# Kernel optimization log

Hardware: AMD Instinct MI355X
Metric: run time of the kernel (lower is better)

## Reference

```python
import jax, jax.numpy as jnp
import numpy as np

T, B, V, L_MAX = 1000, 64, 1024, 64
BLANK = 0
LAMBDA_FAIR = 0.5
NUM_GROUPS = 2
NEG = jnp.float32(-1e30)  # finite stand-in for -inf (nan-safe under vjp)


def setup_inputs() -> dict:
    key = jax.random.key(0)
    k1, k2, k3, k4, k5 = jax.random.split(key, 5)
    # caller passes log-softmaxed acoustic model outputs [T, B, V]
    log_probs = jax.nn.log_softmax(jax.random.normal(k1, (T, B, V), jnp.float32), axis=-1)
    # flat concatenated targets; values in [1, V) (blank=0 excluded, as in real CTC targets)
    targets = jax.random.randint(k2, (B * L_MAX,), 1, V, dtype=jnp.int32)
    input_lengths = jax.random.randint(k3, (B,), T // 2, T + 1, dtype=jnp.int32)
    target_lengths = jax.random.randint(k4, (B,), 0, L_MAX, dtype=jnp.int32)  # 0 allowed (tests t_len==0 branch)
    group_ids = jax.random.randint(k5, (B,), 0, NUM_GROUPS, dtype=jnp.int32)
    return {"log_probs": log_probs, "targets": targets, "input_lengths": input_lengths,
            "target_lengths": target_lengths, "group_ids": group_ids}


def _ctc_per_sample(log_probs, targets, input_lengths, target_lengths):
    """Batched CTC NLL (reduction='none'), log-domain alpha recursion."""
    Tn, Bn, Vn = log_probs.shape
    # unflatten targets per sample: offsets = exclusive cumsum of target_lengths
    offsets = jnp.cumsum(target_lengths) - target_lengths                      # [B]
    pos = offsets[:, None] + jnp.arange(L_MAX)[None, :]                        # [B, L]
    valid = jnp.arange(L_MAX)[None, :] < target_lengths[:, None]
    tgt = jnp.where(valid, targets[jnp.clip(pos, 0, targets.shape[0] - 1)], BLANK)  # [B, L]

    S = 2 * L_MAX + 1  # extended label sequence with interleaved blanks
    ext = jnp.full((Bn, S), BLANK, dtype=targets.dtype).at[:, 1::2].set(tgt)   # [B, S]
    # emission log-probs gathered once: em[t, b, s] = log_probs[t, b, ext[b, s]]
    em = jnp.take_along_axis(log_probs, jnp.broadcast_to(ext[None], (Tn, Bn, S)), axis=2)

    ext_m2 = jnp.pad(ext[:, :-2], ((0, 0), (2, 0)), constant_values=BLANK)
    s_idx = jnp.arange(S)
    allow_skip = (s_idx[None, :] >= 2) & (ext != BLANK) & (ext != ext_m2)      # [B, S]

    def end_ll(alpha):
        last = 2 * target_lengths                                              # index of final blank
        a1 = jnp.take_along_axis(alpha, last[:, None], axis=1)[:, 0]
        a2 = jnp.take_along_axis(alpha, jnp.clip(last - 1, 0)[:, None], axis=1)[:, 0]
        return jnp.logaddexp(a1, jnp.where(target_lengths > 0, a2, NEG))

    alpha0 = jnp.full((Bn, S), NEG).at[:, 0].set(em[0, :, 0])
    alpha0 = alpha0.at[:, 1].set(jnp.where(target_lengths > 0, em[0, :, 1], NEG))
    final0 = jnp.where(input_lengths == 1, end_ll(alpha0), NEG)

    def step(carry, xs):
        alpha, final = carry
        em_t, t = xs
        sh1 = jnp.concatenate([jnp.full((Bn, 1), NEG), alpha[:, :-1]], axis=1)
        sh2 = jnp.concatenate([jnp.full((Bn, 2), NEG), alpha[:, :-2]], axis=1)
        alpha = jnp.logaddexp(jnp.logaddexp(alpha, sh1),
                              jnp.where(allow_skip, sh2, NEG)) + em_t
        final = jnp.where(t == input_lengths - 1, end_ll(alpha), final)
        return (alpha, final), None

    (_, final), _ = jax.lax.scan(step, (alpha0, final0), (em[1:], jnp.arange(1, Tn)))
    loss = jnp.where(target_lengths > 0, -final, 0.0)   # t_len==0 -> loss 0 (as in original)
    loss = jnp.where(loss < 1e29, loss, 0.0)            # zero_infinity=True
    return loss


def reference(log_probs, targets, input_lengths, target_lengths, group_ids):
    per_sample = _ctc_per_sample(log_probs, targets, input_lengths, target_lengths)  # [B]
    base_loss = per_sample.mean()
    ones = jnp.ones_like(per_sample)
    counts = jax.ops.segment_sum(ones, group_ids, num_segments=NUM_GROUPS)
    sums = jax.ops.segment_sum(per_sample, group_ids, num_segments=NUM_GROUPS)
    group_means = sums / jnp.maximum(counts, 1.0)
    fairness_penalty = jnp.var(group_means, ddof=1)     # torch .var() is unbiased
    total = base_loss + LAMBDA_FAIR * fairness_penalty
    return total, base_loss, fairness_penalty
```

## Files before the change

kernel.cpp:

```cpp
#include <hip/hip_runtime.h>

#define T_ 1000
#define B_ 64
#define V_ 1024
#define NEGF (-1e30f)
#define LOG2E_ 1.4426950408889634f
#define LN2_ 0.6931471805599453f
#define P0C 1.4405f
#define P1C (-0.64178f)
#define P2C 0.20128f

__device__ __forceinline__ float ex2(float x) { return __builtin_amdgcn_exp2f(x); }
__device__ __forceinline__ float lg2(float x) { return __builtin_amdgcn_logf(x); }
__device__ __forceinline__ float rlane(float x, int l) {
    return __int_as_float(__builtin_amdgcn_readlane(__float_as_int(x), l));
}
#define FENCE_ __builtin_amdgcn_sched_barrier(0)

__device__ __forceinline__ void load_tgt(const int* __restrict__ targets,
                                         const int* __restrict__ tlen,
                                         int b, int lane, int& tg, int& L) {
    int tl = tlen[lane];
    L = __shfl(tl, b);
    int v = (lane < b) ? tl : 0;
    for (int off = 32; off; off >>= 1) v += __shfl_xor(v, off);
    tg = (lane < L) ? targets[v + lane] : 0;
}

__global__ __launch_bounds__(64) void ctc_fb_k(const float* __restrict__ lp,
                                               const int* __restrict__ targets,
                                               const int* __restrict__ tlen,
                                               const int* __restrict__ ilen,
                                               float* __restrict__ aw) {
    int blk = blockIdx.x, lane = threadIdx.x;
    bool isFwd = blk < B_;
    int b = isFwd ? blk : blk - B_;
    int tg, L;
    load_tgt(targets, tlen, b, lane, tg, L);
    int Tin = ilen[b], Te = Tin - 1;
    int M = Te >> 1;
    int tgp = __shfl_up(tg, 1);
    bool skip1 = (lane >= 1) && (tg != 0) && (tg != tgp);
    int col = (lane == 63) ? 0 : tg;
    int idx = (b << 10) + col;
    float* awb = aw + b * 256;

    if (isFwd) {
        bool is16 = (lane == 16), is32 = (lane == 32), is48 = (lane == 48);
        float a0 = NEGF, a1 = NEGF;
        auto ldG = [&](int g, float4& S) {
            int t0 = 4 * g;
            int ta = t0 < M ? t0 : M, tb2 = t0 + 1 < M ? t0 + 1 : M;
            int tc = t0 + 2 < M ? t0 + 2 : M, td = t0 + 3 < M ? t0 + 3 : M;
            S.x = (lp + ((size_t)ta << 16))[idx];
            S.y = (lp + ((size_t)tb2 << 16))[idx];
            S.z = (lp + ((size_t)tc << 16))[idx];
            S.w = (lp + ((size_t)td << 16))[idx];
        };
        auto shr1 = [&](float x) -> float {
            float v15 = rlane(x, 15), v31 = rlane(x, 31), v47 = rlane(x, 47);
            float bval = is16 ? v15 : (is32 ? v31 : (is48 ? v47 : NEGF));
            return __int_as_float(__builtin_amdgcn_update_dpp(
                __float_as_int(bval), __float_as_int(x), 0x111, 0xF, 0xF, false));
        };
        auto step = [&](float xb, float xe) {
            float p1m = shr1(a1);
            float d0 = a0 - p1m;
            float m0 = fmaxf(a0, p1m);
            float u = ex2(-fabsf(d0));
            float h = fmaf(u, P2C, P1C);
            h = fmaf(u, h, P0C);
            float U = fmaf(u, h, m0);
            float na0 = U + xb;
            float w = skip1 ? U : a0;
            float d1 = a1 - w;
            float m1 = fmaxf(a1, w);
            float v = ex2(-fabsf(d1));
            float h1 = fmaf(v, P2C, P1C);
            h1 = fmaf(v, h1, P0C);
            float na1 = fmaf(v, h1, m1 + xe);
            a0 = na0; a1 = na1;
        };
        if (M >= 35) {
            float4 S0, S1, S2, S3, S4, S5, S6, S7;
            ldG(0, S0); ldG(1, S1); ldG(2, S2); ldG(3, S3);
            ldG(4, S4); ldG(5, S5); ldG(6, S6); ldG(7, S7);
            FENCE_;
            {
                float e0 = S0.x * LOG2E_, e1 = S0.y * LOG2E_;
                float e2 = S0.z * LOG2E_, e3 = S0.w * LOG2E_;
                a0 = (lane == 0) ? rlane(e0, 63) : NEGF;
                a1 = (lane == 0 && L > 0) ? e0 : NEGF;
                step(rlane(e1, 63), e1); step(rlane(e2, 63), e2); step(rlane(e3, 63), e3);
                ldG(8, S0);
                FENCE_;
            }
#define SUBF_F(S, G) do {                                                      \
            float e0_ = S.x * LOG2E_, e1_ = S.y * LOG2E_;                      \
            float e2_ = S.z * LOG2E_, e3_ = S.w * LOG2E_;                      \
            float b0_ = rlane(e0_, 63), b1_ = rlane(e1_, 63);                  \
            float b2_ = rlane(e2_, 63), b3_ = rlane(e3_, 63);                  \
            step(b0_, e0_); step(b1_, e1_); step(b2_, e2_); step(b3_, e3_);    \
            ldG((G) + 8, S);                                                   \
            FENCE_;                                                            \
        } while (0)
            SUBF_F(S1, 1); SUBF_F(S2, 2); SUBF_F(S3, 3); SUBF_F(S4, 4);
            SUBF_F(S5, 5); SUBF_F(S6, 6); SUBF_F(S7, 7);
            int c = 1;
            for (; 32 * c + 31 <= M; ++c) {
                int g0 = 8 * c;
                SUBF_F(S0, g0 + 0); SUBF_F(S1, g0 + 1); SUBF_F(S2, g0 + 2); SUBF_F(S3, g0 + 3);
                SUBF_F(S4, g0 + 4); SUBF_F(S5, g0 + 5); SUBF_F(S6, g0 + 6); SUBF_F(S7, g0 + 7);
            }
#undef SUBF_F
            int tb = 32 * c;
#define SUBT_F(S, T0) do {                                                     \
            float e0_ = S.x * LOG2E_, e1_ = S.y * LOG2E_;                      \
            float e2_ = S.z * LOG2E_, e3_ = S.w * LOG2E_;                      \
            float b0_ = rlane(e0_, 63), b1_ = rlane(e1_, 63);                  \
            float b2_ = rlane(e2_, 63), b3_ = rlane(e3_, 63);                  \
            if ((T0) + 0 <= M) step(b0_, e0_);                                 \
            if ((T0) + 1 <= M) step(b1_, e1_);                                 \
            if ((T0) + 2 <= M) step(b2_, e2_);                                 \
            if ((T0) + 3 <= M) step(b3_, e3_);                                 \
        } while (0)
            SUBT_F(S0, tb + 0);  SUBT_F(S1, tb + 4);  SUBT_F(S2, tb + 8);  SUBT_F(S3, tb + 12);
            SUBT_F(S4, tb + 16); SUBT_F(S5, tb + 20); SUBT_F(S6, tb + 24); SUBT_F(S7, tb + 28);
#undef SUBT_F
        } else if (Tin >= 1) {
            float e = lp[idx] * LOG2E_;
            a0 = (lane == 0) ? rlane(e, 63) : NEGF;
            a1 = (lane == 0 && L > 0) ? e : NEGF;
            for (int t = 1; t <= M; ++t) {
                float xe = (lp + ((size_t)t << 16))[idx] * LOG2E_;
                step(rlane(xe, 63), xe);
            }
        }
        awb[lane] = a0;
        awb[64 + lane] = a1;
    } else {
        bool is15 = (lane == 15), is31 = (lane == 31), is47 = (lane == 47);
        int K = Te - M;
        float B0 = (lane == L) ? 0.0f : NEGF;
        float B1 = (L > 0 && lane == L - 1) ? 0.0f : NEGF;
        auto ldG = [&](int g, float4& S) {
            int t0 = Te - 4 * g;
            int ta = t0 > 0 ? t0 : 0, tb2 = t0 - 1 > 0 ? t0 - 1 : 0;
            int tc = t0 - 2 > 0 ? t0 - 2 : 0, td = t0 - 3 > 0 ? t0 - 3 : 0;
            S.x = (lp + ((size_t)ta << 16))[idx];
            S.y = (lp + ((size_t)tb2 << 16))[idx];
            S.z = (lp + ((size_t)tc << 16))[idx];
            S.w = (lp + ((size_t)td << 16))[idx];
        };
        auto shl1 = [&](float x) -> float {
            float v16 = rlane(x, 16), v32 = rlane(x, 32), v48 = rlane(x, 48);
            float bval = is15 ? v16 : (is31 ? v32 : (is47 ? v48 : NEGF));
            return __int_as_float(__builtin_amdgcn_update_dpp(
                __float_as_int(bval), __float_as_int(x), 0x101, 0xF, 0xF, false));
        };
        auto stepb = [&](float xb, float xe) {
            float z = B1 + xe;
            float t0v = B0 + xb;
            float d0 = t0v - z;
            float m0 = fmaxf(t0v, z);
            float u = ex2(-fabsf(d0));
            float h = fmaf(u, P2C, P1C);
            h = fmaf(u, h, P0C);
            float B0n = fmaf(u, h, m0);
            float y = skip1 ? B0n : t0v;
            float arg = shl1(y);
            float d1 = z - arg;
            float m1 = fmaxf(z, arg);
            float v = ex2(-fabsf(d1));
            float h1 = fmaf(v, P2C, P1C);
            h1 = fmaf(v, h1, P0C);
            float B1n = fmaf(v, h1, m1);
            B0 = B0n; B1 = B1n;
        };
        if (K >= 35) {
            float4 S0, S1, S2, S3, S4, S5, S6, S7;
            ldG(0, S0); ldG(1, S1); ldG(2, S2); ldG(3, S3);
            ldG(4, S4); ldG(5, S5); ldG(6, S6); ldG(7, S7);
            FENCE_;
#define SUBF_B(S, G) do {                                                      \
            float e0_ = S.x * LOG2E_, e1_ = S.y * LOG2E_;                      \
            float e2_ = S.z * LOG2E_, e3_ = S.w * LOG2E_;                      \
            float b0_ = rlane(e0_, 63), b1_ = rlane(e1_, 63);                  \
            float b2_ = rlane(e2_, 63), b3_ = rlane(e3_, 63);                  \
            stepb(b0_, e0_); stepb(b1_, e1_); stepb(b2_, e2_); stepb(b3_, e3_);\
            ldG((G) + 8, S);                                                   \
            FENCE_;                                                            \
        } while (0)
            SUBF_B(S0, 0); SUBF_B(S1, 1); SUBF_B(S2, 2); SUBF_B(S3, 3);
            SUBF_B(S4, 4); SUBF_B(S5, 5); SUBF_B(S6, 6); SUBF_B(S7, 7);
            int c = 1;
            for (; 32 * c + 31 <= K - 1; ++c) {
                int g0 = 8 * c;
                SUBF_B(S0, g0 + 0); SUBF_B(S1, g0 + 1); SUBF_B(S2, g0 + 2); SUBF_B(S3, g0 + 3);
                SUBF_B(S4, g0 + 4); SUBF_B(S5, g0 + 5); SUBF_B(S6, g0 + 6); SUBF_B(S7, g0 + 7);
            }
#undef SUBF_B
            int kb = 32 * c;
#define SUBT_B(S, K0) do {                                                     \
            float e0_ = S.x * LOG2E_, e1_ = S.y * LOG2E_;                      \
            float e2_ = S.z * LOG2E_, e3_ = S.w * LOG2E_;                      \
            float b0_ = rlane(e0_, 63), b1_ = rlane(e1_, 63);                  \
            float b2_ = rlane(e2_, 63), b3_ = rlane(e3_, 63);                  \
            if ((K0) + 0 <= K - 1) stepb(b0_, e0_);                            \
            if ((K0) + 1 <= K - 1) stepb(b1_, e1_);                            \
            if ((K0) + 2 <= K - 1) stepb(b2_, e2_);                            \
            if ((K0) + 3 <= K - 1) stepb(b3_, e3_);                            \
        } while (0)
            SUBT_B(S0, kb + 0);  SUBT_B(S1, kb + 4);  SUBT_B(S2, kb + 8);  SUBT_B(S3, kb + 12);
            SUBT_B(S4, kb + 16); SUBT_B(S5, kb + 20); SUBT_B(S6, kb + 24); SUBT_B(S7, kb + 28);
#undef SUBT_B
        } else {
            for (int k = 0; k < K; ++k) {
                int t = Te - k;
                float xe = (lp + ((size_t)t << 16))[idx] * LOG2E_;
                stepb(rlane(xe, 63), xe);
            }
        }
        awb[128 + lane] = B0;
        awb[192 + lane] = B1;
    }
}

__global__ __launch_bounds__(64) void combine_k(const float* __restrict__ aw,
                                                const int* __restrict__ tlen,
                                                const int* __restrict__ ilen,
                                                float* __restrict__ losses) {
    int b = blockIdx.x, lane = threadIdx.x;
    const float* awb = aw + b * 256;
    float s0 = awb[lane] + awb[128 + lane];
    float s1 = awb[64 + lane] + awb[192 + lane];
    float m = fmaxf(s0, s1);
    for (int off = 32; off; off >>= 1) m = fmaxf(m, __shfl_xor(m, off));
    float sum = ex2(s0 - m) + ex2(s1 - m);
    for (int off = 32; off; off >>= 1) sum += __shfl_xor(sum, off);
    if (lane == 0) {
        int L = tlen[b];
        float fin = lg2(sum) + m;
        if (ilen[b] <= 0) fin = NEGF;
        float loss = (L > 0) ? -fin * LN2_ : 0.0f;
        if (!(loss < 1e29f)) loss = 0.0f;
        losses[b] = loss;
    }
}

__global__ __launch_bounds__(64) void ctc_rec_direct_k(const float* __restrict__ lp,
                                                       const int* __restrict__ targets,
                                                       const int* __restrict__ tlen,
                                                       const int* __restrict__ ilen,
                                                       float* __restrict__ losses) {
    int b = blockIdx.x, lane = threadIdx.x;
    int tg, L;
    load_tgt(targets, tlen, b, lane, tg, L);
    int Tin = ilen[b], Te = Tin - 1;
    int tgp = __shfl_up(tg, 1);
    bool skip1 = (lane >= 1) && (tg != 0) && (tg != tgp);
    bool is16 = (lane == 16), is32 = (lane == 32), is48 = (lane == 48);
    int col = (lane == 63) ? 0 : tg;
    int idx = (b << 10) + col;
    float a0 = NEGF, a1 = NEGF;
    auto shr1 = [&](float x) -> float {
        float v15 = rlane(x, 15), v31 = rlane(x, 31), v47 = rlane(x, 47);
        float bval = is16 ? v15 : (is32 ? v31 : (is48 ? v47 : NEGF));
        return __int_as_float(__builtin_amdgcn_update_dpp(
            __float_as_int(bval), __float_as_int(x), 0x111, 0xF, 0xF, false));
    };
    auto step = [&](float xb, float xe) {
        float p1m = shr1(a1);
        float d0 = a0 - p1m;
        float m0 = fmaxf(a0, p1m);
        float u = ex2(-fabsf(d0));
        float h = fmaf(u, P2C, P1C);
        h = fmaf(u, h, P0C);
        float U = fmaf(u, h, m0);
        float na0 = U + xb;
        float w = skip1 ? U : a0;
        float d1 = a1 - w;
        float m1 = fmaxf(a1, w);
        float v = ex2(-fabsf(d1));
        float h1 = fmaf(v, P2C, P1C);
        h1 = fmaf(v, h1, P0C);
        float na1 = fmaf(v, h1, m1 + xe);
        a0 = na0; a1 = na1;
    };
    if (Tin >= 1) {
        float e = lp[idx] * LOG2E_;
        a0 = (lane == 0) ? rlane(e, 63) : NEGF;
        a1 = (lane == 0 && L > 0) ? e : NEGF;
        for (int t = 1; t <= Te; ++t) {
            float xe = (lp + ((size_t)t << 16))[idx] * LOG2E_;
            step(rlane(xe, 63), xe);
        }
    }
    int lidx = (L > 0) ? (L - 1) : 0;
    float aPrev = __shfl(a1, lidx);
    float aLast = __shfl(a0, (L < 63) ? L : 63);
    float x = aLast, y = (L > 0) ? aPrev : NEGF;
    float m = fmaxf(x, y), d = fminf(x, y) - m;
    float fin = m + lg2(1.0f + ex2(d));
    if (Tin <= 0) fin = NEGF;
    if (lane == 0) {
        float loss = (L > 0) ? -fin * LN2_ : 0.0f;
        if (!(loss < 1e29f)) loss = 0.0f;
        losses[b] = loss;
    }
}

__global__ __launch_bounds__(64) void finalize_k(const float* __restrict__ losses,
                                                 const int* __restrict__ gid,
                                                 float* __restrict__ out) {
    int lane = threadIdx.x;
    float l = losses[lane];
    int g = gid[lane];
    float s = l;
    float s0 = (g == 0) ? l : 0.0f, c0 = (g == 0) ? 1.0f : 0.0f;
    float s1 = (g == 1) ? l : 0.0f, c1 = (g == 1) ? 1.0f : 0.0f;
    for (int off = 32; off; off >>= 1) {
        s  += __shfl_xor(s, off);
        s0 += __shfl_xor(s0, off);
        c0 += __shfl_xor(c0, off);
        s1 += __shfl_xor(s1, off);
        c1 += __shfl_xor(c1, off);
    }
    if (lane == 0) {
        float base = s * (1.0f / B_);
        float m0 = s0 / fmaxf(c0, 1.0f);
        float m1 = s1 / fmaxf(c1, 1.0f);
        float mean = 0.5f * (m0 + m1);
        float var = (m0 - mean) * (m0 - mean) + (m1 - mean) * (m1 - mean);
        out[0] = base + 0.5f * var;
        out[1] = base;
        out[2] = var;
    }
}

extern "C" void kernel_launch(void* const* d_in, const int* in_sizes, int n_in,
                              void* d_out, int out_size, void* d_ws, size_t ws_size,
                              hipStream_t stream) {
    const float* lp = (const float*)d_in[0];
    const int* targets = (const int*)d_in[1];
    const int* ilen = (const int*)d_in[2];
    const int* tlen = (const int*)d_in[3];
    const int* gid = (const int*)d_in[4];
    float* out = (float*)d_out;

    char* ws = (char*)d_ws;
    float* losses = (float*)ws;
    float* aw = (float*)(ws + 1024);
    size_t need = 1024 + (size_t)B_ * 256 * 4;

    if (ws_size >= need) {
        ctc_fb_k<<<2 * B_, 64, 0, stream>>>(lp, targets, tlen, ilen, aw);
        combine_k<<<B_, 64, 0, stream>>>(aw, tlen, ilen, losses);
    } else {
        ctc_rec_direct_k<<<B_, 64, 0, stream>>>(lp, targets, tlen, ilen, losses);
    }
    finalize_k<<<1, 64, 0, stream>>>(losses, gid, out);
}
```

Baseline: 46.78 us.

## Interleave forward and backward CTC recursions in one wavefront per sample

Forward alpha and backward beta recursions, which used to run as separate blocks (2*B waves), now run in a single wavefront per sample with their steps interleaved. The two dependency chains are independent, so interleaving gives the scheduler instruction-level parallelism to hide the latency of exp, DPP and readlane ops within one wave. In exchange it uses half as many waves and roughly doubles register pressure from the two prefetch buffer sets. The tail handling is also more complex when M and K-1 differ.

```diff
diff --git a/kernel.cpp b/kernel.cpp
--- a/kernel.cpp
+++ b/kernel.cpp
@@ -27,203 +27,187 @@
     tg = (lane < L) ? targets[v + lane] : 0;
 }
 
-__global__ __launch_bounds__(64) void ctc_fb_k(const float* __restrict__ lp,
-                                               const int* __restrict__ targets,
-                                               const int* __restrict__ tlen,
-                                               const int* __restrict__ ilen,
-                                               float* __restrict__ aw) {
-    int blk = blockIdx.x, lane = threadIdx.x;
-    bool isFwd = blk < B_;
-    int b = isFwd ? blk : blk - B_;
+__global__ __launch_bounds__(64) void ctc_fb2_k(const float* __restrict__ lp,
+                                                const int* __restrict__ targets,
+                                                const int* __restrict__ tlen,
+                                                const int* __restrict__ ilen,
+                                                float* __restrict__ aw) {
+    int b = blockIdx.x, lane = threadIdx.x;
     int tg, L;
     load_tgt(targets, tlen, b, lane, tg, L);
     int Tin = ilen[b], Te = Tin - 1;
     int M = Te >> 1;
+    int K = Te - M;
     int tgp = __shfl_up(tg, 1);
     bool skip1 = (lane >= 1) && (tg != 0) && (tg != tgp);
     int col = (lane == 63) ? 0 : tg;
     int idx = (b << 10) + col;
     float* awb = aw + b * 256;
 
-    if (isFwd) {
-        bool is16 = (lane == 16), is32 = (lane == 32), is48 = (lane == 48);
-        float a0 = NEGF, a1 = NEGF;
-        auto ldG = [&](int g, float4& S) {
-            int t0 = 4 * g;
-            int ta = t0 < M ? t0 : M, tb2 = t0 + 1 < M ? t0 + 1 : M;
-            int tc = t0 + 2 < M ? t0 + 2 : M, td = t0 + 3 < M ? t0 + 3 : M;
-            S.x = (lp + ((size_t)ta << 16))[idx];
-            S.y = (lp + ((size_t)tb2 << 16))[idx];
-            S.z = (lp + ((size_t)tc << 16))[idx];
-            S.w = (lp + ((size_t)td << 16))[idx];
-        };
-        auto shr1 = [&](float x) -> float {
-            float v15 = rlane(x, 15), v31 = rlane(x, 31), v47 = rlane(x, 47);
-            float bval = is16 ? v15 : (is32 ? v31 : (is48 ? v47 : NEGF));
-            return __int_as_float(__builtin_amdgcn_update_dpp(
-                __float_as_int(bval), __float_as_int(x), 0x111, 0xF, 0xF, false));
-        };
-        auto step = [&](float xb, float xe) {
-            float p1m = shr1(a1);
-            float d0 = a0 - p1m;
-            float m0 = fmaxf(a0, p1m);
-            float u = ex2(-fabsf(d0));
-            float h = fmaf(u, P2C, P1C);
-            h = fmaf(u, h, P0C);
-            float U = fmaf(u, h, m0);
-            float na0 = U + xb;
-            float w = skip1 ? U : a0;
-            float d1 = a1 - w;
-            float m1 = fmaxf(a1, w);
-            float v = ex2(-fabsf(d1));
-            float h1 = fmaf(v, P2C, P1C);
-            h1 = fmaf(v, h1, P0C);
-            float na1 = fmaf(v, h1, m1 + xe);
-            a0 = na0; a1 = na1;
-        };
-        if (M >= 35) {
-            float4 S0, S1, S2, S3, S4, S5, S6, S7;
-            ldG(0, S0); ldG(1, S1); ldG(2, S2); ldG(3, S3);
-            ldG(4, S4); ldG(5, S5); ldG(6, S6); ldG(7, S7);
+    bool is16 = (lane == 16), is32 = (lane == 32), is48 = (lane == 48);
+    bool is15 = (lane == 15), is31 = (lane == 31), is47 = (lane == 47);
+
+    float a0 = NEGF, a1 = NEGF;
+    float B0 = (lane == L) ? 0.0f : NEGF;
+    float B1 = (L > 0 && lane == L - 1) ? 0.0f : NEGF;
+
+    auto ldF = [&](int g, float4& S) {
+        int t0 = 4 * g;
+        int ta = t0 < M ? t0 : M, tb2 = t0 + 1 < M ? t0 + 1 : M;
+        int tc = t0 + 2 < M ? t0 + 2 : M, td = t0 + 3 < M ? t0 + 3 : M;
+        S.x = (lp + ((size_t)ta << 16))[idx];
+        S.y = (lp + ((size_t)tb2 << 16))[idx];
+        S.z = (lp + ((size_t)tc << 16))[idx];
+        S.w = (lp + ((size_t)td << 16))[idx];
+    };
+    auto ldB = [&](int g, float4& S) {
+        int t0 = Te - 4 * g;
+        int ta = t0 > 0 ? t0 : 0, tb2 = t0 - 1 > 0 ? t0 - 1 : 0;
+        int tc = t0 - 2 > 0 ? t0 - 2 : 0, td = t0 - 3 > 0 ? t0 - 3 : 0;
+        S.x = (lp + ((size_t)ta << 16))[idx];
+        S.y = (lp + ((size_t)tb2 << 16))[idx];
+        S.z = (lp + ((size_t)tc << 16))[idx];
+        S.w = (lp + ((size_t)td << 16))[idx];
+    };
+    auto shr1 = [&](float x) -> float {
+        float v15 = rlane(x, 15), v31 = rlane(x, 31), v47 = rlane(x, 47);
+        float bval = is16 ? v15 : (is32 ? v31 : (is48 ? v47 : NEGF));
+        return __int_as_float(__builtin_amdgcn_update_dpp(
+            __float_as_int(bval), __float_as_int(x), 0x111, 0xF, 0xF, false));
+    };
+    auto shl1 = [&](float x) -> float {
+        float v16 = rlane(x, 16), v32 = rlane(x, 32), v48 = rlane(x, 48);
+        float bval = is15 ? v16 : (is31 ? v32 : (is47 ? v48 : NEGF));
+        return __int_as_float(__builtin_amdgcn_update_dpp(
+            __float_as_int(bval), __float_as_int(x), 0x101, 0xF, 0xF, false));
+    };
+    auto step = [&](float xb, float xe) {
+        float p1m = shr1(a1);
+        float d0 = a0 - p1m;
+        float m0 = fmaxf(a0, p1m);
+        float u = ex2(-fabsf(d0));
+        float h = fmaf(u, P2C, P1C);
+        h = fmaf(u, h, P0C);
+        float U = fmaf(u, h, m0);
+        float na0 = U + xb;
+        float w = skip1 ? U : a0;
+        float d1 = a1 - w;
+        float m1 = fmaxf(a1, w);
+        float v = ex2(-fabsf(d1));
+        float h1 = fmaf(v, P2C, P1C);
+        h1 = fmaf(v, h1, P0C);
+        float na1 = fmaf(v, h1, m1 + xe);
+        a0 = na0; a1 = na1;
+    };
+    auto stepb = [&](float xb, float xe) {
+        float z = B1 + xe;
+        float t0v = B0 + xb;
+        float d0 = t0v - z;
+        float m0 = fmaxf(t0v, z);
+        float u = ex2(-fabsf(d0));
+        float h = fmaf(u, P2C, P1C);
+        h = fmaf(u, h, P0C);
+        float B0n = fmaf(u, h, m0);
+        float y = skip1 ? B0n : t0v;
+        float arg = shl1(y);
+        float d1 = z - arg;
+        float m1 = fmaxf(z, arg);
+        float v = ex2(-fabsf(d1));
+        float h1 = fmaf(v, P2C, P1C);
+        h1 = fmaf(v, h1, P0C);
+        float B1n = fmaf(v, h1, m1);
+        B0 = B0n; B1 = B1n;
+    };
+
+    if (M >= 35) {
+        float4 F0, F1, F2, F3, F4, F5, F6, F7;
+        float4 R0, R1, R2, R3, R4, R5, R6, R7;
+        ldF(0, F0); ldB(0, R0); ldF(1, F1); ldB(1, R1);
+        ldF(2, F2); ldB(2, R2); ldF(3, F3); ldB(3, R3);
+        ldF(4, F4); ldB(4, R4); ldF(5, F5); ldB(5, R5);
+        ldF(6, F6); ldB(6, R6); ldF(7, F7); ldB(7, R7);
+        FENCE_;
+        {
+            float f0 = F0.x * LOG2E_, f1 = F0.y * LOG2E_;
+            float f2 = F0.z * LOG2E_, f3 = F0.w * LOG2E_;
+            float g0 = R0.x * LOG2E_, g1 = R0.y * LOG2E_;
+            float g2 = R0.z * LOG2E_, g3 = R0.w * LOG2E_;
+            a0 = (lane == 0) ? rlane(f0, 63) : NEGF;
+            a1 = (lane == 0 && L > 0) ? f0 : NEGF;
+            step(rlane(f1, 63), f1); stepb(rlane(g0, 63), g0);
+            step(rlane(f2, 63), f2); stepb(rlane(g1, 63), g1);
+            step(rlane(f3, 63), f3); stepb(rlane(g2, 63), g2);
+            stepb(rlane(g3, 63), g3);
+            ldF(8, F0); ldB(8, R0);
             FENCE_;
-            {
-                float e0 = S0.x * LOG2E_, e1 = S0.y * LOG2E_;
-                float e2 = S0.z * LOG2E_, e3 = S0.w * LOG2E_;
-                a0 = (lane == 0) ? rlane(e0, 63) : NEGF;
-                a1 = (lane == 0 && L > 0) ? e0 : NEGF;
-                step(rlane(e1, 63), e1); step(rlane(e2, 63), e2); step(rlane(e3, 63), e3);
-                ldG(8, S0);
-                FENCE_;
-            }
-#define SUBF_F(S, G) do {                                                      \
-            float e0_ = S.x * LOG2E_, e1_ = S.y * LOG2E_;                      \
-            float e2_ = S.z * LOG2E_, e3_ = S.w * LOG2E_;                      \
-            float b0_ = rlane(e0_, 63), b1_ = rlane(e1_, 63);                  \
-            float b2_ = rlane(e2_, 63), b3_ = rlane(e3_, 63);                  \
-            step(b0_, e0_); step(b1_, e1_); step(b2_, e2_); step(b3_, e3_);    \
-            ldG((G) + 8, S);                                                   \
-            FENCE_;                                                            \
-        } while (0)
-            SUBF_F(S1, 1); SUBF_F(S2, 2); SUBF_F(S3, 3); SUBF_F(S4, 4);
-            SUBF_F(S5, 5); SUBF_F(S6, 6); SUBF_F(S7, 7);
-            int c = 1;
-            for (; 32 * c + 31 <= M; ++c) {
-                int g0 = 8 * c;
-                SUBF_F(S0, g0 + 0); SUBF_F(S1, g0 + 1); SUBF_F(S2, g0 + 2); SUBF_F(S3, g0 + 3);
-                SUBF_F(S4, g0 + 4); SUBF_F(S5, g0 + 5); SUBF_F(S6, g0 + 6); SUBF_F(S7, g0 + 7);
-            }
-#undef SUBF_F
-            int tb = 32 * c;
-#define SUBT_F(S, T0) do {                                                     \
-            float e0_ = S.x * LOG2E_, e1_ = S.y * LOG2E_;                      \
-            float e2_ = S.z * LOG2E_, e3_ = S.w * LOG2E_;                      \
-            float b0_ = rlane(e0_, 63), b1_ = rlane(e1_, 63);                  \
-            float b2_ = rlane(e2_, 63), b3_ = rlane(e3_, 63);                  \
-            if ((T0) + 0 <= M) step(b0_, e0_);                                 \
-            if ((T0) + 1 <= M) step(b1_, e1_);                                 \
-            if ((T0) + 2 <= M) step(b2_, e2_);                                 \
-            if ((T0) + 3 <= M) step(b3_, e3_);                                 \
-        } while (0)
-            SUBT_F(S0, tb + 0);  SUBT_F(S1, tb + 4);  SUBT_F(S2, tb + 8);  SUBT_F(S3, tb + 12);
-            SUBT_F(S4, tb + 16); SUBT_F(S5, tb + 20); SUBT_F(S6, tb + 24); SUBT_F(S7, tb + 28);
-#undef SUBT_F
-        } else if (Tin >= 1) {
-            float e = lp[idx] * LOG2E_;
-            a0 = (lane == 0) ? rlane(e, 63) : NEGF;
-            a1 = (lane == 0 && L > 0) ? e : NEGF;
-            for (int t = 1; t <= M; ++t) {
-                float xe = (lp + ((size_t)t << 16))[idx] * LOG2E_;
-                step(rlane(xe, 63), xe);
-            }
-        }
-        awb[lane] = a0;
-        awb[64 + lane] = a1;
-    } else {
-        bool is15 = (lane == 15), is31 = (lane == 31), is47 = (lane == 47);
-        int K = Te - M;
-        float B0 = (lane == L) ? 0.0f : NEGF;
-        float B1 = (L > 0 && lane == L - 1) ? 0.0f : NEGF;
-        auto ldG = [&](int g, float4& S) {
-            int t0 = Te - 4 * g;
-            int ta = t0 > 0 ? t0 : 0, tb2 = t0 - 1 > 0 ? t0 - 1 : 0;
-            int tc = t0 - 2 > 0 ? t0 - 2 : 0, td = t0 - 3 > 0 ? t0 - 3 : 0;
-            S.x = (lp + ((size_t)ta << 16))[idx];
-            S.y = (lp + ((size_t)tb2 << 16))[idx];
-            S.z = (lp + ((size_t)tc << 16))[idx];
-            S.w = (lp + ((size_t)td << 16))[idx];
-        };
-        auto shl1 = [&](float x) -> float {
-            float v16 = rlane(x, 16), v32 = rlane(x, 32), v48 = rlane(x, 48);
-            float bval = is15 ? v16 : (is31 ? v32 : (is47 ? v48 : NEGF));
-            return __int_as_float(__builtin_amdgcn_update_dpp(
-                __float_as_int(bval), __float_as_int(x), 0x101, 0xF, 0xF, false));
-        };
-        auto stepb = [&](float xb, float xe) {
-            float z = B1 + xe;
-            float t0v = B0 + xb;
-            float d0 = t0v - z;
-            float m0 = fmaxf(t0v, z);
-            float u = ex2(-fabsf(d0));
-            float h = fmaf(u, P2C, P1C);
-            h = fmaf(u, h, P0C);
-            float B0n = fmaf(u, h, m0);
-            float y = skip1 ? B0n : t0v;
-            float arg = shl1(y);
-            float d1 = z - arg;
-            float m1 = fmaxf(z, arg);
-            float v = ex2(-fabsf(d1));
-            float h1 = fmaf(v, P2C, P1C);
-            h1 = fmaf(v, h1, P0C);
-            float B1n = fmaf(v, h1, m1);
-            B0 = B0n; B1 = B1n;
-        };
-        if (K >= 35) {
-            float4 S0, S1, S2, S3, S4, S5, S6, S7;
-            ldG(0, S0); ldG(1, S1); ldG(2, S2); ldG(3, S3);
-            ldG(4, S4); ldG(5, S5); ldG(6, S6); ldG(7, S7);
-            FENCE_;
-#define SUBF_B(S, G) do {                                                      \
-            float e0_ = S.x * LOG2E_, e1_ = S.y * LOG2E_;                      \
-            float e2_ = S.z * LOG2E_, e3_ = S.w * LOG2E_;                      \
-            float b0_ = rlane(e0_, 63), b1_ = rlane(e1_, 63);                  \
-            float b2_ = rlane(e2_, 63), b3_ = rlane(e3_, 63);                  \
-            stepb(b0_, e0_); stepb(b1_, e1_); stepb(b2_, e2_); stepb(b3_, e3_);\
-            ldG((G) + 8, S);                                                   \
-            FENCE_;                                                            \
-        } while (0)
-            SUBF_B(S0, 0); SUBF_B(S1, 1); SUBF_B(S2, 2); SUBF_B(S3, 3);
-            SUBF_B(S4, 4); SUBF_B(S5, 5); SUBF_B(S6, 6); SUBF_B(S7, 7);
-            int c = 1;
-            for (; 32 * c + 31 <= K - 1; ++c) {
-                int g0 = 8 * c;
-                SUBF_B(S0, g0 + 0); SUBF_B(S1, g0 + 1); SUBF_B(S2, g0 + 2); SUBF_B(S3, g0 + 3);
-                SUBF_B(S4, g0 + 4); SUBF_B(S5, g0 + 5); SUBF_B(S6, g0 + 6); SUBF_B(S7, g0 + 7);
-            }
-#undef SUBF_B
-            int kb = 32 * c;
-#define SUBT_B(S, K0) do {                                                     \
-            float e0_ = S.x * LOG2E_, e1_ = S.y * LOG2E_;                      \
-            float e2_ = S.z * LOG2E_, e3_ = S.w * LOG2E_;                      \
-            float b0_ = rlane(e0_, 63), b1_ = rlane(e1_, 63);                  \
-            float b2_ = rlane(e2_, 63), b3_ = rlane(e3_, 63);                  \
-            if ((K0) + 0 <= K - 1) stepb(b0_, e0_);                            \
-            if ((K0) + 1 <= K - 1) stepb(b1_, e1_);                            \
-            if ((K0) + 2 <= K - 1) stepb(b2_, e2_);                            \
-            if ((K0) + 3 <= K - 1) stepb(b3_, e3_);                            \
-        } while (0)
-            SUBT_B(S0, kb + 0);  SUBT_B(S1, kb + 4);  SUBT_B(S2, kb + 8);  SUBT_B(S3, kb + 12);
-            SUBT_B(S4, kb + 16); SUBT_B(S5, kb + 20); SUBT_B(S6, kb + 24); SUBT_B(S7, kb + 28);
-#undef SUBT_B
-        } else {
-            for (int k = 0; k < K; ++k) {
-                int t = Te - k;
-                float xe = (lp + ((size_t)t << 16))[idx] * LOG2E_;
-                stepb(rlane(xe, 63), xe);
-            }
-        }
-        awb[128 + lane] = B0;
-        awb[192 + lane] = B1;
-    }
+        }
+#define COMB(F, R, G) do {                                                     \
+        float f0_ = F.x * LOG2E_, f1_ = F.y * LOG2E_;                          \
+        float f2_ = F.z * LOG2E_, f3_ = F.w * LOG2E_;                          \
+        float g0_ = R.x * LOG2E_, g1_ = R.y * LOG2E_;                          \
+        float g2_ = R.z * LOG2E_, g3_ = R.w * LOG2E_;                          \
+        float fb0_ = rlane(f0_, 63), fb1_ = rlane(f1_, 63);                    \
+        float fb2_ = rlane(f2_, 63), fb3_ = rlane(f3_, 63);                    \
+        float gb0_ = rlane(g0_, 63), gb1_ = rlane(g1_, 63);                    \
+        float gb2_ = rlane(g2_, 63), gb3_ = rlane(g3_, 63);                    \
+        step(fb0_, f0_); stepb(gb0_, g0_);                                     \
+        step(fb1_, f1_); stepb(gb1_, g1_);                                     \
+        step(fb2_, f2_); stepb(gb2_, g2_);                                     \
+        step(fb3_, f3_); stepb(gb3_, g3_);                                     \
+        ldF((G) + 8, F); ldB((G) + 8, R);                                      \
+        FENCE_;                                                                \
+    } while (0)
+        COMB(F1, R1, 1); COMB(F2, R2, 2); COMB(F3, R3, 3);
+        COMB(F4, R4, 4); COMB(F5, R5, 5); COMB(F6, R6, 6); COMB(F7, R7, 7);
+        int mn = (M < K - 1) ? M : (K - 1);
+        int c = 1;
+        for (; 32 * c + 31 <= mn; ++c) {
+            int g0 = 8 * c;
+            COMB(F0, R0, g0 + 0); COMB(F1, R1, g0 + 1);
+            COMB(F2, R2, g0 + 2); COMB(F3, R3, g0 + 3);
+            COMB(F4, R4, g0 + 4); COMB(F5, R5, g0 + 5);
+            COMB(F6, R6, g0 + 6); COMB(F7, R7, g0 + 7);
+        }
+#undef COMB
+        int tb = 32 * c;
+#define TAILC(F, R, T0) do {                                                   \
+        float f0_ = F.x * LOG2E_, f1_ = F.y * LOG2E_;                          \
+        float f2_ = F.z * LOG2E_, f3_ = F.w * LOG2E_;                          \
+        float g0_ = R.x * LOG2E_, g1_ = R.y * LOG2E_;                          \
+        float g2_ = R.z * LOG2E_, g3_ = R.w * LOG2E_;                          \
+        if ((T0) + 0 <= M) step(rlane(f0_, 63), f0_);                          \
+        if ((T0) + 0 <= K - 1) stepb(rlane(g0_, 63), g0_);                     \
+        if ((T0) + 1 <= M) step(rlane(f1_, 63), f1_);                          \
+        if ((T0) + 1 <= K - 1) stepb(rlane(g1_, 63), g1_);                     \
+        if ((T0) + 2 <= M) step(rlane(f2_, 63), f2_);                          \
+        if ((T0) + 2 <= K - 1) stepb(rlane(g2_, 63), g2_);                     \
+        if ((T0) + 3 <= M) step(rlane(f3_, 63), f3_);                          \
+        if ((T0) + 3 <= K - 1) stepb(rlane(g3_, 63), g3_);                     \
+    } while (0)
+        TAILC(F0, R0, tb + 0);  TAILC(F1, R1, tb + 4);
+        TAILC(F2, R2, tb + 8);  TAILC(F3, R3, tb + 12);
+        TAILC(F4, R4, tb + 16); TAILC(F5, R5, tb + 20);
+        TAILC(F6, R6, tb + 24); TAILC(F7, R7, tb + 28);
+#undef TAILC
+    } else if (Tin >= 1) {
+        float e = lp[idx] * LOG2E_;
+        a0 = (lane == 0) ? rlane(e, 63) : NEGF;
+        a1 = (lane == 0 && L > 0) ? e : NEGF;
+        for (int t = 1; t <= M; ++t) {
+            float xe = (lp + ((size_t)t << 16))[idx] * LOG2E_;
+            step(rlane(xe, 63), xe);
+        }
+        for (int k = 0; k < K; ++k) {
+            int t = Te - k;
+            float xe = (lp + ((size_t)t << 16))[idx] * LOG2E_;
+            stepb(rlane(xe, 63), xe);
+        }
+    }
+
+    awb[lane] = a0;
+    awb[64 + lane] = a1;
+    awb[128 + lane] = B0;
+    awb[192 + lane] = B1;
 }
 
 __global__ __launch_bounds__(64) void combine_k(const float* __restrict__ aw,
@@ -354,7 +338,7 @@
     size_t need = 1024 + (size_t)B_ * 256 * 4;
 
     if (ws_size >= need) {
-        ctc_fb_k<<<2 * B_, 64, 0, stream>>>(lp, targets, tlen, ilen, aw);
+        ctc_fb2_k<<<B_, 64, 0, stream>>>(lp, targets, tlen, ilen, aw);
         combine_k<<<B_, 64, 0, stream>>>(aw, tlen, ilen, losses);
     } else {
         ctc_rec_direct_k<<<B_, 64, 0, stream>>>(lp, targets, tlen, ilen, losses);
```

New measurement: 78.88 us. +68.6%, slower.
